# Optimization experiments

Hardware: AMD Instinct MI355X
Metric: run time of the kernel (lower is better)

## Reference

```python
import jax, jax.numpy as jnp
import numpy as np
import math

A = 32; B = 32; PSIZE = 16; K = 3; STRIDE = 2; PAD = 1; ITERS = 3; FINAL_LAMBDA = 0.01
KK = K * K; KKA = KK * A; KKA2 = KKA // 2 + 1
EPS = 1e-12; LN2PI = math.log(2 * math.pi)


def unfold(x, k, s, p):
    # torch F.unfold: output feature dim ordered (C, kh, kw), columns row-major
    b, C, h, w = x.shape
    xp = jnp.pad(x, ((0, 0), (0, 0), (p, p), (p, p)))
    oh = (h + 2 * p - k) // s + 1
    ow = (w + 2 * p - k) // s + 1
    cols = [xp[:, :, ki:ki + s * (oh - 1) + 1:s, kj:kj + s * (ow - 1) + 1:s]
            for ki in range(k) for kj in range(k)]
    patches = jnp.stack(cols, axis=2)  # [b, C, kk, oh, ow]
    return patches.reshape(b, C, k * k, oh * ow), oh, ow


def setup_inputs():
    key = jax.random.key(0)
    ks = jax.random.split(key, 8)
    b, h, w = 4, 14, 14
    a_in = jax.random.uniform(ks[0], (b, A, h, w), dtype=jnp.float32)
    pose = jax.random.normal(ks[1], (b, A * PSIZE, h, w), dtype=jnp.float32)
    mpose_w = jax.random.normal(ks[2], (B * PSIZE, PSIZE), dtype=jnp.float32) / np.float32(np.sqrt(PSIZE))
    mpose_b = jnp.zeros((B * PSIZE,), jnp.float32)
    freq_w = jax.random.normal(ks[3], (KKA2, PSIZE, 2), dtype=jnp.float32) * 0.02
    ln_g = jnp.ones((A,), jnp.float32)
    ln_b = jnp.zeros((A,), jnp.float32)
    lim = np.float32(np.sqrt(6.0 / (KK + KK)))  # xavier_uniform on [kk, kk, 1]
    spat_w = jax.random.uniform(ks[4], (KK, KK, 1), jnp.float32, -lim, lim)
    spat_bias = jnp.ones((KK,), jnp.float32)
    beta_u = jnp.zeros((1, 1, B, 1), jnp.float32)
    beta_a = jnp.zeros((1, 1, B), jnp.float32)
    return dict(a_in=a_in, pose=pose, mpose_w=mpose_w, mpose_b=mpose_b,
                freq_w=freq_w, ln_g=ln_g, ln_b=ln_b, spat_w=spat_w,
                spat_bias=spat_bias, beta_u=beta_u, beta_a=beta_a)


def _forward(a_in, pose, mpose_w, mpose_b, freq_w, ln_g, ln_b,
             spat_w, spat_bias, beta_u, beta_a):
    b = a_in.shape[0]
    pose_u, oh, ow = unfold(pose, K, STRIDE, PAD)  # [b, A*PSIZE, KK, l]
    l = oh * ow
    pose_u = pose_u.reshape(b, A, PSIZE, KK, l)
    pose_u = pose_u.transpose(0, 4, 3, 1, 2).reshape(b, l, KKA, PSIZE)
    # mpose linear: psize -> B*psize
    po = jnp.einsum('blkp,qp->blkq', pose_u, mpose_w) + mpose_b
    po = po.reshape(b * l, KKA, B, PSIZE)
    # Frequency FFT filter over kkA axis (weight shared across all B slices)
    xf = jnp.fft.rfft(po, axis=1, norm='ortho')        # [bl, KKA2, B, PSIZE] complex
    wc = freq_w[..., 0] + 1j * freq_w[..., 1]           # [KKA2, PSIZE]
    xf = xf * wc[None, :, None, :]
    po = jnp.fft.irfft(xf, n=KKA, axis=1, norm='ortho') + po  # residual
    v = po.reshape(b, l, KKA, B, PSIZE)
    a_u, _, _ = unfold(a_in, K, STRIDE, PAD)            # [b, A, KK, l]
    a_u = a_u.transpose(0, 3, 2, 1).reshape(b, l, KKA)
    # Spatial gating applied to ones-initialized r (identical for every B slice)
    ones = jnp.ones((b * l, KKA), jnp.float32)
    g = ones.reshape(b * l, KK, A)
    mu_g = g.mean(-1, keepdims=True)
    var_g = ((g - mu_g) ** 2).mean(-1, keepdims=True)
    gn = (g - mu_g) / jnp.sqrt(var_g + 1e-5) * ln_g + ln_b
    g2 = jnp.einsum('ij,nja->nia', spat_w[:, :, 0], gn) + spat_bias[None, :, None]
    gate = jax.nn.gelu(g2, approximate=False).reshape(b * l, KKA) + ones
    logit = jnp.broadcast_to(gate[:, :, None], (b * l, KKA, B))
    r = jax.nn.softmax(logit, axis=2).reshape(b, l, KKA, B, 1)
    a_out = mu = None
    for i in range(ITERS):
        lam = FINAL_LAMBDA * (1.0 - 0.95 ** (i + 1))
        # m-step
        rr = r * a_u[:, :, :, None, None]
        r_sum = rr.sum(axis=2, keepdims=True)                 # [b,l,1,B,1]
        coeff = rr / (r_sum + EPS)
        mu = (coeff * v).sum(axis=2, keepdims=True)           # [b,l,1,B,PSIZE]
        sig = (coeff * (v - mu) ** 2).sum(axis=2, keepdims=True) + EPS
        cost = (beta_u + jnp.log(jnp.sqrt(sig[:, :, 0]))) * r_sum[:, :, 0]  # [b,l,B,PSIZE]
        a_out = jax.nn.sigmoid(lam * (beta_a - cost.sum(axis=3)))           # [b,l,B]
        if i < ITERS - 1:
            # e-step (note: log(sigma_sq * ln2pi) is faithful to the original code)
            ln_p = (-0.5 * jnp.sum(jnp.log(sig * LN2PI), axis=-1)
                    - jnp.sum((v - mu) ** 2 / (2.0 * sig), axis=-1))        # [b,l,KKA,B]
            ln_ap = ln_p + jnp.log(a_out[:, :, None, :])
            r = jax.nn.softmax(ln_ap, axis=-1)[..., None]
    pose_out = mu[:, :, 0].reshape(b, l, B * PSIZE).transpose(0, 2, 1).reshape(b, B * PSIZE, oh, ow)
    a_fin = a_out.transpose(0, 2, 1).reshape(b, B, oh, ow)
    return a_fin, pose_out


def reference(a_in, pose, mpose_w, mpose_b, freq_w, ln_g, ln_b,
              spat_w, spat_bias, beta_u, beta_a):
    return _forward(a_in, pose, mpose_w, mpose_b, freq_w, ln_g, ln_b,
                    spat_w, spat_bias, beta_u, beta_a)
```

## Files before the change

kernel.cpp:

```cpp
#include <hip/hip_runtime.h>
#include <hip/hip_bf16.h>
#include <math.h>

#define A_    32
#define B_    32
#define PS    16
#define KK_   9
#define KKA_  288
#define OH_   7
#define L_    49
#define NB    4
#define NSITE 196
#define NCOLS 3136

#define LAM1 5.0e-4f
#define LAM2 9.75e-4f
#define LAM3 1.42625e-3f
#define LOG_LN2PI 0.6086775903077413f

typedef _Float16 half2v __attribute__((ext_vector_type(2)));
typedef short    short8 __attribute__((ext_vector_type(8)));
typedef float    floatx4 __attribute__((ext_vector_type(4)));

static __device__ __forceinline__ float san(float x, float lo, float hi){
    return fminf(fmaxf(x, lo), hi);
}

static __device__ __forceinline__ float dot2acc(half2v a, half2v b, float c){
#if __has_builtin(__builtin_amdgcn_fdot2)
    return __builtin_amdgcn_fdot2(a, b, c, false);
#else
    return c + (float)a.x*(float)b.x + (float)a.y*(float)b.y;
#endif
}

__global__ void k_prep(const float* __restrict__ fw, const float* __restrict__ pose,
                       ushort* __restrict__ cpr, float* __restrict__ csum,
                       __hip_bfloat16* __restrict__ Xt, int nc)
{
    if ((int)blockIdx.x < nc){
        int id = (int)blockIdx.x*256 + threadIdx.x;
        if (id >= 16*288) return;
        int p = id / 288, m = id % 288;
        float acc = fw[(0*16 + p)*2 + 0];
        for (int k = 1; k <= 143; ++k){
            float re = fw[(k*16 + p)*2 + 0];
            float im = fw[(k*16 + p)*2 + 1];
            int km = (k*m) % 288;
            float ang = 0.021816615649929116f * (float)km;
            float s, c; __sincosf(ang, &s, &c);
            acc += 2.0f*(re*c - im*s);
        }
        float re144 = fw[(144*16 + p)*2 + 0];
        acc += re144 * ((m & 1) ? -1.0f : 1.0f);
        float cv = acc * (1.0f/288.0f);
        if (m == 0) cv += 1.0f;
        cv = san(cv, -1e4f, 1e4f);

        __hip_bfloat16 hb = __float2bfloat16(cv);
        float hif = __bfloat162float(hb);
        __hip_bfloat16 lb = __float2bfloat16(cv - hif);
        ushort hi = *(ushort*)&hb, lo = *(ushort*)&lb;

        ushort* c0h = cpr + p*592;
        ushort* c1h = cpr + 16*592   + p*592;
        ushort* c0l = cpr + 16*592*2 + p*592;
        ushort* c1l = cpr + 16*592*3 + p*592;
        int x1 = 288 - m;
        c0h[x1] = hi;  c0l[x1] = lo;
        c1h[x1-1] = hi; c1l[x1-1] = lo;
        if (m >= 1){
            int x2 = 576 - m;
            c0h[x2] = hi;  c0l[x2] = lo;
            c1h[x2-1] = hi; c1l[x2-1] = lo;
        } else {
            c0h[0] = hi; c0l[0] = lo;
            csum[p] = san(1.0f + fw[(0*16 + p)*2 + 0], -1e4f, 1e4f);
        }
        return;
    }
    int id = ((int)blockIdx.x - nc)*256 + threadIdx.x;
    if (id >= NCOLS*KKA_) return;
    int c = id / KKA_, j = id % KKA_;
    int n = c >> 4, q = c & 15;
    int bs = n / L_, l = n % L_, oy = l / OH_, ox = l % OH_;
    int kk = j >> 5, a = j & 31;
    int y = oy*2 - 1 + kk/3, x = ox*2 - 1 + kk%3;
    float v = 0.f;
    if ((unsigned)y < 14u && (unsigned)x < 14u)
        v = pose[((bs*(A_*PS) + a*PS + q)*14 + y)*14 + x];
    Xt[id] = __float2bfloat16(san(v, -1e4f, 1e4f));
}

__launch_bounds__(512, 1)
__global__ void
k_mega(const ushort* __restrict__ cpr, const __hip_bfloat16* __restrict__ Xt,
       const float* __restrict__ a_in,
       const float* __restrict__ mpw, const float* __restrict__ mpb,
       const float* __restrict__ csum,
       const float* __restrict__ beta_u, const float* __restrict__ beta_a,
       float* __restrict__ out)
{
    const int nl = blockIdx.x;
    const int t = threadIdx.x;
    const int Bc = t >> 4, p = t & 15;
    const int bs = nl / L_, l = nl % L_;

    __shared__ uint      v_lds[72][512];
    __shared__ _Float16  us[16*264];
    __shared__ float     a_s[KKA_];
    __shared__ float     d_s[16][33];
    __shared__ float     rbuf[16][33];
    __shared__ float     cst[32];

    for (int j = t; j < KKA_; j += 512){
        int kk = j >> 5, a = j & 31;
        int oy = l / OH_, ox = l % OH_;
        int y = oy*2 - 1 + kk/3, x = ox*2 - 1 + kk%3;
        float v = 0.f;
        if ((unsigned)y < 14u && (unsigned)x < 14u)
            v = a_in[((bs*A_ + a)*14 + y)*14 + x];
        a_s[j] = san(v, 0.f, 1e4f);
    }
    half2v w_h[8];
    #pragma unroll
    for (int k = 0; k < 8; ++k){
        w_h[k].x = (_Float16)mpw[t*16 + 2*k];
        w_h[k].y = (_Float16)mpw[t*16 + 2*k + 1];
    }
    const float vb = mpb[t] * csum[p];
    const float bu = beta_u[Bc];
    const float ba = beta_a[Bc];
    __syncthreads();

    float S0tot = 0.f;
    for (int j = 0; j < KKA_; ++j) S0tot += a_s[j];

    const int w = t >> 6, lane = t & 63;
    const int mn = lane & 15, quad = lane >> 4;
    const int p0 = w*2;
    const __hip_bfloat16* xrow = Xt + (nl*16 + mn)*KKA_ + quad*8;

    float S1 = 0.f, S2 = 0.f;
    half2v v_h[72];

    for (int ch = 0; ch < 9; ++ch){
        floatx4 accA = {0,0,0,0}, accB = {0,0,0,0};
        for (int k0i = 0; k0i < 9; ++k0i){
            const int k0 = k0i*32;
            short8 bfrag = *(const short8*)&xrow[k0];
            #pragma unroll
            for (int pp = 0; pp < 2; ++pp){
                const int pg = p0 + pp;
                int o = 288 + k0 + quad*8 - (ch*16 + mn);
                int sel = o & 1, off = o - sel;
                const ushort* bh = cpr + (sel ? 16*592 : 0) + pg*592;
                const ushort* bl = cpr + 16*592*2 + (sel ? 16*592 : 0) + pg*592;
                short8 ah = *(const short8*)&bh[off];
                short8 al = *(const short8*)&bl[off];
                floatx4 acc = pp ? accB : accA;
                acc = __builtin_amdgcn_mfma_f32_16x16x32_bf16(ah, bfrag, acc, 0, 0, 0);
                acc = __builtin_amdgcn_mfma_f32_16x16x32_bf16(al, bfrag, acc, 0, 0, 0);
                if (pp) accB = acc; else accA = acc;
            }
        }
        #pragma unroll
        for (int r = 0; r < 4; ++r){
            us[p0*264     + (quad*4 + r)*16 + mn] = (_Float16)accA[r];
            us[(p0+1)*264 + (quad*4 + r)*16 + mn] = (_Float16)accB[r];
        }
        __syncthreads();
        const _Float16* urow = &us[p*264];
        #pragma unroll
        for (int s = 0; s < 8; ++s){
            const int i0 = ch*16 + 2*s;
            union { uint4 u4; half2v h2[4]; } A0, A1, B0, B1;
            A0.u4 = *(const uint4*)&urow[(2*s)*16];
            A1.u4 = *(const uint4*)&urow[(2*s)*16 + 8];
            B0.u4 = *(const uint4*)&urow[(2*s+1)*16];
            B1.u4 = *(const uint4*)&urow[(2*s+1)*16 + 8];
            float v0 = vb, v1 = vb;
            #pragma unroll
            for (int m = 0; m < 4; ++m){
                v0 = dot2acc(A0.h2[m], w_h[m],   v0);
                v0 = dot2acc(A1.h2[m], w_h[4+m], v0);
                v1 = dot2acc(B0.h2[m], w_h[m],   v1);
                v1 = dot2acc(B1.h2[m], w_h[4+m], v1);
            }
            const float a0 = a_s[i0], a1 = a_s[i0+1];
            S1 += a0*v0 + a1*v1;
            S2 += a0*v0*v0 + a1*v1*v1;
            union { half2v h; uint u; } cv;
            cv.h.x = (_Float16)v0; cv.h.y = (_Float16)v1;
            v_lds[ch*8 + s][t] = cv.u;
        }
        __syncthreads();
    }
    #pragma unroll
    for (int c2 = 0; c2 < 9; ++c2){
        const int ch = 9 + c2;
        floatx4 accA = {0,0,0,0}, accB = {0,0,0,0};
        for (int k0i = 0; k0i < 9; ++k0i){
            const int k0 = k0i*32;
            short8 bfrag = *(const short8*)&xrow[k0];
            #pragma unroll
            for (int pp = 0; pp < 2; ++pp){
                const int pg = p0 + pp;
                int o = 288 + k0 + quad*8 - (ch*16 + mn);
                int sel = o & 1, off = o - sel;
                const ushort* bh = cpr + (sel ? 16*592 : 0) + pg*592;
                const ushort* bl = cpr + 16*592*2 + (sel ? 16*592 : 0) + pg*592;
                short8 ah = *(const short8*)&bh[off];
                short8 al = *(const short8*)&bl[off];
                floatx4 acc = pp ? accB : accA;
                acc = __builtin_amdgcn_mfma_f32_16x16x32_bf16(ah, bfrag, acc, 0, 0, 0);
                acc = __builtin_amdgcn_mfma_f32_16x16x32_bf16(al, bfrag, acc, 0, 0, 0);
                if (pp) accB = acc; else accA = acc;
            }
        }
        #pragma unroll
        for (int r = 0; r < 4; ++r){
            us[p0*264     + (quad*4 + r)*16 + mn] = (_Float16)accA[r];
            us[(p0+1)*264 + (quad*4 + r)*16 + mn] = (_Float16)accB[r];
        }
        __syncthreads();
        const _Float16* urow = &us[p*264];
        #pragma unroll
        for (int s = 0; s < 8; ++s){
            const int i0 = ch*16 + 2*s;
            union { uint4 u4; half2v h2[4]; } A0, A1, B0, B1;
            A0.u4 = *(const uint4*)&urow[(2*s)*16];
            A1.u4 = *(const uint4*)&urow[(2*s)*16 + 8];
            B0.u4 = *(const uint4*)&urow[(2*s+1)*16];
            B1.u4 = *(const uint4*)&urow[(2*s+1)*16 + 8];
            float v0 = vb, v1 = vb;
            #pragma unroll
            for (int m = 0; m < 4; ++m){
                v0 = dot2acc(A0.h2[m], w_h[m],   v0);
                v0 = dot2acc(A1.h2[m], w_h[4+m], v0);
                v1 = dot2acc(B0.h2[m], w_h[m],   v1);
                v1 = dot2acc(B1.h2[m], w_h[4+m], v1);
            }
            const float a0 = a_s[i0], a1 = a_s[i0+1];
            S1 += a0*v0 + a1*v1;
            S2 += a0*v0*v0 + a1*v1*v1;
            half2v vh; vh.x = (_Float16)v0; vh.y = (_Float16)v1;
            v_h[c2*8 + s] = vh;
        }
        __syncthreads();
    }

    float mu_r, i2s_r;
    {
        const float rs  = S0tot * (1.0f/32.0f);
        const float inv = 1.0f / (rs + 1e-12f);
        const float S1r = S1 * (1.0f/32.0f), S2r = S2 * (1.0f/32.0f);
        mu_r = S1r * inv;
        const float sg  = fmaxf((S2r - 2.f*mu_r*S1r + mu_r*mu_r*rs) * inv, 0.f) + 1e-12f;
        i2s_r = 0.5f / sg;
        const float lg  = logf(sg);
        float cs = (bu + 0.5f*lg) * rs;
        float ls = lg + LOG_LN2PI;
        #pragma unroll
        for (int m = 1; m < 16; m <<= 1){ cs += __shfl_xor(cs, m, 16); ls += __shfl_xor(ls, m, 16); }
        const float aout = san(1.f/(1.f + expf(-LAM1*(ba - cs))), 1e-30f, 1.f);
        if (p == 0) cst[Bc] = logf(aout) - 0.5f*ls;
    }
    __syncthreads();

    const int b0 = p & 1, b1 = (p>>1)&1, b2 = (p>>2)&1, b3 = (p>>3)&1;
    float muF = 0.f, aF = 0.f;
    for (int it = 0; it < 2; ++it){
        const float lam = it ? LAM3 : LAM2;
        float T0 = 0.f, T1 = 0.f, T2 = 0.f;

        auto process = [&](int ibase, auto getpair){
            float e1[8], e2[4], e3[2], dfin;
            #pragma unroll
            for (int s = 0; s < 8; ++s){
                float v0, v1; getpair(s, v0, v1);
                float d0 = v0 - mu_r, d1 = v1 - mu_r;
                float ea = d0*d0*i2s_r, eb = d1*d1*i2s_r;
                float aown  = b0 ? eb : ea;
                float asend = b0 ? ea : eb;
                e1[s] = aown + __shfl_xor(asend, 1);
            }
            #pragma unroll
            for (int s = 0; s < 4; ++s){
                float aown  = b1 ? e1[2*s+1] : e1[2*s];
                float asend = b1 ? e1[2*s]   : e1[2*s+1];
                e2[s] = aown + __shfl_xor(asend, 2);
            }
            #pragma unroll
            for (int s = 0; s < 2; ++s){
                float aown  = b2 ? e2[2*s+1] : e2[2*s];
                float asend = b2 ? e2[2*s]   : e2[2*s+1];
                e3[s] = aown + __shfl_xor(asend, 4);
            }
            {
                float aown  = b3 ? e3[1] : e3[0];
                float asend = b3 ? e3[0] : e3[1];
                dfin = aown + __shfl_xor(asend, 8);
            }
            d_s[p][Bc] = dfin;
            __syncthreads();
            {
                const int isub = t >> 5, Bce = t & 31;
                float lnap = cst[Bce] - d_s[isub][Bce];
                float mx = lnap;
                #pragma unroll
                for (int m = 16; m >= 1; m >>= 1) mx = fmaxf(mx, __shfl_xor(mx, m));
                float ex = expf(lnap - mx);
                float sm = ex;
                #pragma unroll
                for (int m = 16; m >= 1; m >>= 1) sm += __shfl_xor(sm, m);
                rbuf[isub][Bce] = (ex / sm) * a_s[ibase + isub];
            }
            __syncthreads();
            #pragma unroll
            for (int s = 0; s < 8; ++s){
                float v0, v1; getpair(s, v0, v1);
                float r0 = rbuf[2*s][Bc], r1 = rbuf[2*s+1][Bc];
                T0 += r0 + r1;
                T1 += r0*v0 + r1*v1;
                T2 += r0*v0*v0 + r1*v1*v1;
            }
        };

        for (int ch = 0; ch < 9; ++ch){
            process(ch*16, [&](int s, float& v0, float& v1){
                union { uint u; half2v h; } cv; cv.u = v_lds[ch*8 + s][t];
                v0 = (float)cv.h.x; v1 = (float)cv.h.y;
            });
        }
        #pragma unroll
        for (int ch = 0; ch < 9; ++ch){
            process(144 + ch*16, [&](int s, float& v0, float& v1){
                half2v vh = v_h[ch*8 + s];
                v0 = (float)vh.x; v1 = (float)vh.y;
            });
        }

        const float inv = 1.f/(T0 + 1e-12f);
        const float mu  = T1 * inv;
        const float sg  = fmaxf((T2 - 2.f*mu*T1 + mu*mu*T0) * inv, 0.f) + 1e-12f;
        const float lg  = logf(sg);
        float cs = (bu + 0.5f*lg) * T0;
        float ls = lg + LOG_LN2PI;
        #pragma unroll
        for (int m = 1; m < 16; m <<= 1){ cs += __shfl_xor(cs, m, 16); ls += __shfl_xor(ls, m, 16); }
        const float aout = san(1.f/(1.f + expf(-lam*(ba - cs))), 1e-30f, 1.f);
        if (it == 0){
            mu_r = mu; i2s_r = 0.5f/sg;
            if (p == 0) cst[Bc] = logf(aout) - 0.5f*ls;
            __syncthreads();
        } else { muF = mu; aF = aout; }
    }

    if (p == 0) out[bs*(B_*L_) + Bc*L_ + l] = san(aF, 0.f, 1.f);
    out[6272 + (bs*512 + t)*L_ + l] = san(muF, -1e4f, 1e4f);
}

extern "C" void kernel_launch(void* const* d_in, const int* in_sizes, int n_in,
                              void* d_out, int out_size, void* d_ws, size_t ws_size,
                              hipStream_t stream)
{
    const float* a_in   = (const float*)d_in[0];
    const float* pose   = (const float*)d_in[1];
    const float* mpw    = (const float*)d_in[2];
    const float* mpb    = (const float*)d_in[3];
    const float* fw     = (const float*)d_in[4];
    const float* beta_u = (const float*)d_in[9];
    const float* beta_a = (const float*)d_in[10];
    float* out = (float*)d_out;

    char* base = (char*)d_ws;
    float*  csum = (float*)(base + 0);
    ushort* cpr  = (ushort*)(base + 256);
    __hip_bfloat16* Xt = (__hip_bfloat16*)(base + 76288);

    const int nc = 18;
    const int nx = (NCOLS*KKA_ + 255)/256;
    k_prep<<<nc + nx, 256, 0, stream>>>(fw, pose, cpr, csum, Xt, nc);
    k_mega<<<NSITE, 512, 0, stream>>>(cpr, Xt, a_in, mpw, mpb, csum, beta_u, beta_a, out);
}
```

Before: 250.3 us.

## Double-buffer chunk scratch, batch E-step softmax, hoist X fragments into registers

The MFMA output buffer is now double-buffered, which removes one barrier per chunk in the M-step loop. The distance tree for all 18 chunks is written to one shared scratch array, followed by a single batched softmax pass and a single accumulation pass. This replaces two barriers per chunk in each E-step iteration with two per iteration. The X fragments are loaded once into registers instead of being reloaded per chunk, and more v values are kept in registers (88 vs 72), with the LDS spill area shrunk to match. The cost is higher register pressure, which risks spilling at 512 threads.

```diff
diff --git a/kernel.cpp b/kernel.cpp
--- a/kernel.cpp
+++ b/kernel.cpp
@@ -106,12 +106,12 @@
     const int Bc = t >> 4, p = t & 15;
     const int bs = nl / L_, l = nl % L_;
 
-    __shared__ uint      v_lds[72][512];
-    __shared__ _Float16  us[16*264];
-    __shared__ float     a_s[KKA_];
-    __shared__ float     d_s[16][33];
-    __shared__ float     rbuf[16][33];
-    __shared__ float     cst[32];
+    __shared__ uint v_lds[56][512];
+    __shared__ __align__(16) float scratch[9792];
+    __shared__ float a_s[KKA_];
+    __shared__ float cst[32];
+
+    float* const dall = scratch;
 
     for (int j = t; j < KKA_; j += 512){
         int kk = j >> 5, a = j & 31;
@@ -131,24 +131,33 @@
     const float vb = mpb[t] * csum[p];
     const float bu = beta_u[Bc];
     const float ba = beta_a[Bc];
-    __syncthreads();
-
-    float S0tot = 0.f;
-    for (int j = 0; j < KKA_; ++j) S0tot += a_s[j];
 
     const int w = t >> 6, lane = t & 63;
     const int mn = lane & 15, quad = lane >> 4;
     const int p0 = w*2;
-    const __hip_bfloat16* xrow = Xt + (nl*16 + mn)*KKA_ + quad*8;
+
+    short8 bf[9];
+    {
+        const __hip_bfloat16* xrow = Xt + (nl*16 + mn)*KKA_ + quad*8;
+        #pragma unroll
+        for (int k = 0; k < 9; ++k) bf[k] = *(const short8*)&xrow[k*32];
+    }
+    __syncthreads();
+
+    float s0a = 0.f, s0b = 0.f, s0c = 0.f, s0d = 0.f;
+    for (int j = 0; j < KKA_; j += 4){
+        s0a += a_s[j]; s0b += a_s[j+1]; s0c += a_s[j+2]; s0d += a_s[j+3];
+    }
+    const float S0tot = (s0a + s0b) + (s0c + s0d);
 
     float S1 = 0.f, S2 = 0.f;
-    half2v v_h[72];
-
-    for (int ch = 0; ch < 9; ++ch){
+    half2v v_h[88];
+
+    auto do_chunk = [&](int ch, _Float16* usb){
         floatx4 accA = {0,0,0,0}, accB = {0,0,0,0};
         for (int k0i = 0; k0i < 9; ++k0i){
             const int k0 = k0i*32;
-            short8 bfrag = *(const short8*)&xrow[k0];
+            short8 bfrag = bf[k0i];
             #pragma unroll
             for (int pp = 0; pp < 2; ++pp){
                 const int pg = p0 + pp;
@@ -166,27 +175,37 @@
         }
         #pragma unroll
         for (int r = 0; r < 4; ++r){
-            us[p0*264     + (quad*4 + r)*16 + mn] = (_Float16)accA[r];
-            us[(p0+1)*264 + (quad*4 + r)*16 + mn] = (_Float16)accB[r];
-        }
+            usb[p0*264     + (quad*4 + r)*16 + mn] = (_Float16)accA[r];
+            usb[(p0+1)*264 + (quad*4 + r)*16 + mn] = (_Float16)accB[r];
+        }
+    };
+
+    auto vpair = [&](const _Float16* urow, int s, float& v0o, float& v1o){
+        union { uint4 u4; half2v h2[4]; } A0, A1, B0, B1;
+        A0.u4 = *(const uint4*)&urow[(2*s)*16];
+        A1.u4 = *(const uint4*)&urow[(2*s)*16 + 8];
+        B0.u4 = *(const uint4*)&urow[(2*s+1)*16];
+        B1.u4 = *(const uint4*)&urow[(2*s+1)*16 + 8];
+        float v0 = vb, v1 = vb;
+        #pragma unroll
+        for (int m = 0; m < 4; ++m){
+            v0 = dot2acc(A0.h2[m], w_h[m],   v0);
+            v0 = dot2acc(A1.h2[m], w_h[4+m], v0);
+            v1 = dot2acc(B0.h2[m], w_h[m],   v1);
+            v1 = dot2acc(B1.h2[m], w_h[4+m], v1);
+        }
+        v0o = v0; v1o = v1;
+    };
+
+    for (int ch = 0; ch < 7; ++ch){
+        _Float16* usb = ((_Float16*)scratch) + (ch & 1)*4224;
+        do_chunk(ch, usb);
         __syncthreads();
-        const _Float16* urow = &us[p*264];
+        const _Float16* urow = &usb[p*264];
         #pragma unroll
         for (int s = 0; s < 8; ++s){
+            float v0, v1; vpair(urow, s, v0, v1);
             const int i0 = ch*16 + 2*s;
-            union { uint4 u4; half2v h2[4]; } A0, A1, B0, B1;
-            A0.u4 = *(const uint4*)&urow[(2*s)*16];
-            A1.u4 = *(const uint4*)&urow[(2*s)*16 + 8];
-            B0.u4 = *(const uint4*)&urow[(2*s+1)*16];
-            B1.u4 = *(const uint4*)&urow[(2*s+1)*16 + 8];
-            float v0 = vb, v1 = vb;
-            #pragma unroll
-            for (int m = 0; m < 4; ++m){
-                v0 = dot2acc(A0.h2[m], w_h[m],   v0);
-                v0 = dot2acc(A1.h2[m], w_h[4+m], v0);
-                v1 = dot2acc(B0.h2[m], w_h[m],   v1);
-                v1 = dot2acc(B1.h2[m], w_h[4+m], v1);
-            }
             const float a0 = a_s[i0], a1 = a_s[i0+1];
             S1 += a0*v0 + a1*v1;
             S2 += a0*v0*v0 + a1*v1*v1;
@@ -194,60 +213,24 @@
             cv.h.x = (_Float16)v0; cv.h.y = (_Float16)v1;
             v_lds[ch*8 + s][t] = cv.u;
         }
+    }
+    #pragma unroll
+    for (int c2 = 0; c2 < 11; ++c2){
+        const int ch = 7 + c2;
+        _Float16* usb = ((_Float16*)scratch) + (ch & 1)*4224;
+        do_chunk(ch, usb);
         __syncthreads();
-    }
-    #pragma unroll
-    for (int c2 = 0; c2 < 9; ++c2){
-        const int ch = 9 + c2;
-        floatx4 accA = {0,0,0,0}, accB = {0,0,0,0};
-        for (int k0i = 0; k0i < 9; ++k0i){
-            const int k0 = k0i*32;
-            short8 bfrag = *(const short8*)&xrow[k0];
-            #pragma unroll
-            for (int pp = 0; pp < 2; ++pp){
-                const int pg = p0 + pp;
-                int o = 288 + k0 + quad*8 - (ch*16 + mn);
-                int sel = o & 1, off = o - sel;
-                const ushort* bh = cpr + (sel ? 16*592 : 0) + pg*592;
-                const ushort* bl = cpr + 16*592*2 + (sel ? 16*592 : 0) + pg*592;
-                short8 ah = *(const short8*)&bh[off];
-                short8 al = *(const short8*)&bl[off];
-                floatx4 acc = pp ? accB : accA;
-                acc = __builtin_amdgcn_mfma_f32_16x16x32_bf16(ah, bfrag, acc, 0, 0, 0);
-                acc = __builtin_amdgcn_mfma_f32_16x16x32_bf16(al, bfrag, acc, 0, 0, 0);
-                if (pp) accB = acc; else accA = acc;
-            }
-        }
-        #pragma unroll
-        for (int r = 0; r < 4; ++r){
-            us[p0*264     + (quad*4 + r)*16 + mn] = (_Float16)accA[r];
-            us[(p0+1)*264 + (quad*4 + r)*16 + mn] = (_Float16)accB[r];
-        }
-        __syncthreads();
-        const _Float16* urow = &us[p*264];
+        const _Float16* urow = &usb[p*264];
         #pragma unroll
         for (int s = 0; s < 8; ++s){
+            float v0, v1; vpair(urow, s, v0, v1);
             const int i0 = ch*16 + 2*s;
-            union { uint4 u4; half2v h2[4]; } A0, A1, B0, B1;
-            A0.u4 = *(const uint4*)&urow[(2*s)*16];
-            A1.u4 = *(const uint4*)&urow[(2*s)*16 + 8];
-            B0.u4 = *(const uint4*)&urow[(2*s+1)*16];
-            B1.u4 = *(const uint4*)&urow[(2*s+1)*16 + 8];
-            float v0 = vb, v1 = vb;
-            #pragma unroll
-            for (int m = 0; m < 4; ++m){
-                v0 = dot2acc(A0.h2[m], w_h[m],   v0);
-                v0 = dot2acc(A1.h2[m], w_h[4+m], v0);
-                v1 = dot2acc(B0.h2[m], w_h[m],   v1);
-                v1 = dot2acc(B1.h2[m], w_h[4+m], v1);
-            }
             const float a0 = a_s[i0], a1 = a_s[i0+1];
             S1 += a0*v0 + a1*v1;
             S2 += a0*v0*v0 + a1*v1*v1;
             half2v vh; vh.x = (_Float16)v0; vh.y = (_Float16)v1;
             v_h[c2*8 + s] = vh;
         }
-        __syncthreads();
     }
 
     float mu_r, i2s_r;
@@ -269,12 +252,12 @@
     __syncthreads();
 
     const int b0 = p & 1, b1 = (p>>1)&1, b2 = (p>>2)&1, b3 = (p>>3)&1;
+    const int isub = t >> 5, Bce = t & 31;
     float muF = 0.f, aF = 0.f;
     for (int it = 0; it < 2; ++it){
         const float lam = it ? LAM3 : LAM2;
-        float T0 = 0.f, T1 = 0.f, T2 = 0.f;
-
-        auto process = [&](int ibase, auto getpair){
+
+        auto dtree = [&](int ibase, auto getpair){
             float e1[8], e2[4], e3[2], dfin;
             #pragma unroll
             for (int s = 0; s < 8; ++s){
@@ -302,11 +285,26 @@
                 float asend = b3 ? e3[0] : e3[1];
                 dfin = aown + __shfl_xor(asend, 8);
             }
-            d_s[p][Bc] = dfin;
-            __syncthreads();
-            {
-                const int isub = t >> 5, Bce = t & 31;
-                float lnap = cst[Bce] - d_s[isub][Bce];
+            dall[(ibase + p)*34 + Bc] = dfin;
+        };
+        #pragma unroll
+        for (int g = 0; g < 7; ++g)
+            dtree(g*16, [&](int s, float& v0, float& v1){
+                union { uint u; half2v h; } cv; cv.u = v_lds[g*8 + s][t];
+                v0 = (float)cv.h.x; v1 = (float)cv.h.y; });
+        #pragma unroll
+        for (int c2 = 0; c2 < 11; ++c2)
+            dtree((7+c2)*16, [&](int s, float& v0, float& v1){
+                half2v vh = v_h[c2*8 + s];
+                v0 = (float)vh.x; v1 = (float)vh.y; });
+        __syncthreads();
+
+        {
+            const float cb = cst[Bce];
+            #pragma unroll
+            for (int g = 0; g < 18; ++g){
+                float* dp = &dall[(g*16 + isub)*34 + Bce];
+                float lnap = cb - *dp;
                 float mx = lnap;
                 #pragma unroll
                 for (int m = 16; m >= 1; m >>= 1) mx = fmaxf(mx, __shfl_xor(mx, m));
@@ -314,32 +312,33 @@
                 float sm = ex;
                 #pragma unroll
                 for (int m = 16; m >= 1; m >>= 1) sm += __shfl_xor(sm, m);
-                rbuf[isub][Bce] = (ex / sm) * a_s[ibase + isub];
-            }
-            __syncthreads();
+                *dp = (ex / sm) * a_s[g*16 + isub];
+            }
+        }
+        __syncthreads();
+
+        float T0 = 0.f, T1 = 0.f, T2 = 0.f;
+        auto csum3 = [&](int ibase, auto getpair){
             #pragma unroll
             for (int s = 0; s < 8; ++s){
                 float v0, v1; getpair(s, v0, v1);
-                float r0 = rbuf[2*s][Bc], r1 = rbuf[2*s+1][Bc];
+                float r0 = dall[(ibase + 2*s)*34 + Bc];
+                float r1 = dall[(ibase + 2*s + 1)*34 + Bc];
                 T0 += r0 + r1;
                 T1 += r0*v0 + r1*v1;
                 T2 += r0*v0*v0 + r1*v1*v1;
             }
         };
-
-        for (int ch = 0; ch < 9; ++ch){
-            process(ch*16, [&](int s, float& v0, float& v1){
-                union { uint u; half2v h; } cv; cv.u = v_lds[ch*8 + s][t];
-                v0 = (float)cv.h.x; v1 = (float)cv.h.y;
-            });
-        }
-        #pragma unroll
-        for (int ch = 0; ch < 9; ++ch){
-            process(144 + ch*16, [&](int s, float& v0, float& v1){
-                half2v vh = v_h[ch*8 + s];
-                v0 = (float)vh.x; v1 = (float)vh.y;
-            });
-        }
+        #pragma unroll
+        for (int g = 0; g < 7; ++g)
+            csum3(g*16, [&](int s, float& v0, float& v1){
+                union { uint u; half2v h; } cv; cv.u = v_lds[g*8 + s][t];
+                v0 = (float)cv.h.x; v1 = (float)cv.h.y; });
+        #pragma unroll
+        for (int c2 = 0; c2 < 11; ++c2)
+            csum3((7+c2)*16, [&](int s, float& v0, float& v1){
+                half2v vh = v_h[c2*8 + s];
+                v0 = (float)vh.x; v1 = (float)vh.y; });
 
         const float inv = 1.f/(T0 + 1e-12f);
         const float mu  = T1 * inv;
```

After: 260.1 us. 3.9% more time.
